# Optimization experiments

Measured on AMD Instinct MI355X. Metric: run time of the kernel, lower is better.

Reference implementation:

```python
import jax, jax.numpy as jnp
import numpy as np

N_HIDDEN = 100  # module-level global n_hidden in source
LN_EPS = 1e-5


def _layernorm(x, g, b):
    mu = jnp.mean(x, axis=-1, keepdims=True)
    var = jnp.mean(jnp.square(x - mu), axis=-1, keepdims=True)
    return (x - mu) * jax.lax.rsqrt(var + LN_EPS) * g + b


def setup_inputs() -> dict:
    key = jax.random.key(0)
    B, T, C, H = 8, 1024, 768, 12
    D = C // H  # head_size = 64
    ks = jax.random.split(key, 12)
    s_qkv = 1.0 / np.sqrt(C)
    s_ff1 = 1.0 / np.sqrt(C)
    s_ff2 = 1.0 / np.sqrt(N_HIDDEN)
    return {
        "x": jax.random.normal(ks[0], (B, T, C), dtype=jnp.float32),
        # per-head K/Q/V projections stacked: [H, C, D]
        "Wq": jax.random.uniform(ks[1], (H, C, D), jnp.float32, -s_qkv, s_qkv),
        "Wk": jax.random.uniform(ks[2], (H, C, D), jnp.float32, -s_qkv, s_qkv),
        "Wv": jax.random.uniform(ks[3], (H, C, D), jnp.float32, -s_qkv, s_qkv),
        "Wproj": jax.random.uniform(ks[4], (C, C), jnp.float32, -s_qkv, s_qkv),
        "bproj": jnp.zeros((C,), jnp.float32),
        "ln1_g": jnp.ones((C,), jnp.float32),
        "ln1_b": jnp.zeros((C,), jnp.float32),
        "W1": jax.random.uniform(ks[5], (C, N_HIDDEN), jnp.float32, -s_ff1, s_ff1),
        "b1": jnp.zeros((N_HIDDEN,), jnp.float32),
        "W2": jax.random.uniform(ks[6], (N_HIDDEN, C), jnp.float32, -s_ff2, s_ff2),
        "b2": jnp.zeros((C,), jnp.float32),
        "ln2_g": jnp.ones((C,), jnp.float32),
        "ln2_b": jnp.zeros((C,), jnp.float32),
    }


def reference(x, Wq, Wk, Wv, Wproj, bproj, ln1_g, ln1_b, W1, b1, W2, b2, ln2_g, ln2_b):
    B, T, C = x.shape
    # batched-over-heads QKV (source does a Python loop per head; same math)
    q = jnp.einsum('btc,hcd->bhtd', x, Wq)
    k = jnp.einsum('btc,hcd->bhtd', x, Wk)
    v = jnp.einsum('btc,hcd->bhtd', x, Wv)
    # NOTE: source scales by C**-0.5 where C = n_embd (not head_size)
    wei = jnp.einsum('bhtd,bhsd->bhts', q, k) * (C ** -0.5)
    wei = jax.nn.softmax(wei, axis=-1)  # attn_maps, returned
    out = jnp.einsum('bhts,bhsd->bhtd', wei, v)
    out = out.transpose(0, 2, 1, 3).reshape(B, T, C)  # concat heads
    attn_out = out @ Wproj + bproj
    h = _layernorm(x + attn_out, ln1_g, ln1_b)
    ff = jax.nn.relu(h @ W1 + b1) @ W2 + b2
    y = _layernorm(h + ff, ln2_g, ln2_b)
    return (wei, y)
```

## Files before the change

### kernel.cpp

```cpp
#include <hip/hip_runtime.h>
#include <hip/hip_bf16.h>
#include <cstdint>

typedef __bf16 bf16_t;
typedef __bf16 bf16x8 __attribute__((ext_vector_type(8)));
typedef __bf16 bf16x4 __attribute__((ext_vector_type(4)));
typedef float f32x4 __attribute__((ext_vector_type(4)));

#define B_ 8
#define T_ 1024
#define C_ 768
#define H_ 12
#define D_ 64
#define NTOK 8192
#define NHID_PAD 128
#define SCALE 0.03608439182435161f
#define WEI_ELEMS 100663296ull

__device__ __forceinline__ f32x4 mfma16(bf16x8 a, bf16x8 b, f32x4 c) {
    return __builtin_amdgcn_mfma_f32_16x16x32_bf16(a, b, c, 0, 0, 0);
}

typedef const unsigned int __attribute__((address_space(1)))* gaddr_t;
typedef unsigned int __attribute__((address_space(3)))* laddr_t;
__device__ __forceinline__ void gload16(const bf16_t* g, bf16_t* l) {
    __builtin_amdgcn_global_load_lds((gaddr_t)g, (laddr_t)l, 16, 0, 0);
}

__global__ __launch_bounds__(256) void k_cast_x(const float* __restrict__ x,
                                                bf16_t* __restrict__ xb) {
    int i = blockIdx.x * 256 + threadIdx.x;
    const float4 v = reinterpret_cast<const float4*>(x)[i];
    bf16x4 o;
    o.x = (bf16_t)v.x; o.y = (bf16_t)v.y; o.z = (bf16_t)v.z; o.w = (bf16_t)v.w;
    *reinterpret_cast<bf16x4*>(xb + 4 * i) = o;
}

__global__ __launch_bounds__(256) void k_pack_qkv(const float* __restrict__ Wq,
                                                  const float* __restrict__ Wk,
                                                  const float* __restrict__ Wv,
                                                  bf16_t* __restrict__ out) {
    int idx = blockIdx.x * 256 + threadIdx.x;
    int row = idx / C_, c = idx - row * C_;
    int p = row / C_;
    int hd = row - p * C_;
    int h = hd >> 6, d = hd & 63;
    const float* W = (p == 0) ? Wq : (p == 1 ? Wk : Wv);
    out[idx] = (bf16_t)W[((size_t)h * C_ + c) * D_ + d];
}

__global__ __launch_bounds__(256) void k_pack_proj(const float* __restrict__ W,
                                                   bf16_t* __restrict__ out) {
    int idx = blockIdx.x * 256 + threadIdx.x;
    int n = idx / C_, k = idx - n * C_;
    out[idx] = (bf16_t)W[(size_t)k * C_ + n];
}

__global__ __launch_bounds__(256) void k_pack_w1(const float* __restrict__ W,
                                                 bf16_t* __restrict__ out) {
    int idx = blockIdx.x * 256 + threadIdx.x;
    int n = idx / C_, k = idx - n * C_;
    out[idx] = (bf16_t)((n < 100) ? W[(size_t)k * 100 + n] : 0.0f);
}

__global__ __launch_bounds__(256) void k_pack_w2(const float* __restrict__ W,
                                                 bf16_t* __restrict__ out) {
    int idx = blockIdx.x * 256 + threadIdx.x;
    int n = idx / NHID_PAD, k = idx & (NHID_PAD - 1);
    out[idx] = (bf16_t)((k < 100) ? W[(size_t)k * C_ + n] : 0.0f);
}

__device__ __forceinline__ void gemm_core(const bf16_t* __restrict__ A, int lda,
                                          const bf16_t* __restrict__ B, int ldb,
                                          int K, f32x4 acc[4][4]) {
    __shared__ __align__(16) bf16_t As[128 * 32];
    __shared__ __align__(16) bf16_t Bs[128 * 32];
    const int tid = threadIdx.x;
    const int wave = tid >> 6, lane = tid & 63;
    const int q = lane >> 4, ln = lane & 15;
    const int wm = (wave >> 1) * 64, wn = (wave & 1) * 64;
    const size_t bm = (size_t)blockIdx.y * 128, bn = (size_t)blockIdx.x * 128;

    const int c0 = wave * 2;
    const int srow = c0 * 16 + (lane >> 2);
    const int kg = (lane & 3) * 8;
    const bf16_t* Ap0 = A + (bm + srow) * lda + kg;
    const bf16_t* Ap1 = A + (bm + srow + 16) * lda + kg;
    const bf16_t* Bp0 = B + (bn + srow) * ldb + kg;
    const bf16_t* Bp1 = B + (bn + srow + 16) * ldb + kg;
    bf16_t* AsD0 = As + c0 * 512;
    bf16_t* AsD1 = As + (c0 + 1) * 512;
    bf16_t* BsD0 = Bs + c0 * 512;
    bf16_t* BsD1 = Bs + (c0 + 1) * 512;

    for (int k0 = 0; k0 < K; k0 += 32) {
        __syncthreads();
        gload16(Ap0 + k0, AsD0);
        gload16(Ap1 + k0, AsD1);
        gload16(Bp0 + k0, BsD0);
        gload16(Bp1 + k0, BsD1);
        __syncthreads();
        bf16x8 af[4], bfr[4];
#pragma unroll
        for (int i = 0; i < 4; ++i)
            af[i] = *reinterpret_cast<const bf16x8*>(&As[(wm + i * 16 + ln) * 32 + q * 8]);
#pragma unroll
        for (int j = 0; j < 4; ++j)
            bfr[j] = *reinterpret_cast<const bf16x8*>(&Bs[(wn + j * 16 + ln) * 32 + q * 8]);
#pragma unroll
        for (int i = 0; i < 4; ++i)
#pragma unroll
            for (int j = 0; j < 4; ++j)
                acc[i][j] = mfma16(af[i], bfr[j], acc[i][j]);
    }
}

#define EPI_PROLOG                                              \
    const int lane = threadIdx.x & 63;                          \
    const int wave = threadIdx.x >> 6;                          \
    const int q = lane >> 4, ln = lane & 15;                    \
    const int row0 = blockIdx.y * 128 + (wave >> 1) * 64;       \
    const int col0 = blockIdx.x * 128 + (wave & 1) * 64;

__global__ __launch_bounds__(256) void k_gemm_qk(const bf16_t* __restrict__ A,
                                                 const bf16_t* __restrict__ Bm,
                                                 bf16_t* __restrict__ qb,
                                                 bf16_t* __restrict__ kb) {
    f32x4 acc[4][4] = {};
    gemm_core(A, C_, Bm, C_, C_, acc);
    EPI_PROLOG
#pragma unroll
    for (int i = 0; i < 4; ++i)
#pragma unroll
        for (int j = 0; j < 4; ++j)
#pragma unroll
            for (int r = 0; r < 4; ++r) {
                int grow = row0 + i * 16 + q * 4 + r;
                int gcol = col0 + j * 16 + ln;
                int p = (gcol >= C_) ? 1 : 0;
                int c = gcol - p * C_;
                int h = c >> 6, d = c & 63;
                int b = grow >> 10, t = grow & 1023;
                bf16_t* dst = p ? kb : qb;
                dst[(((size_t)b * H_ + h) * T_ + t) * D_ + d] = (bf16_t)acc[i][j][r];
            }
}

__global__ __launch_bounds__(256) void k_gemm_vt(const bf16_t* __restrict__ A,
                                                 const bf16_t* __restrict__ Bm,
                                                 bf16_t* __restrict__ vt) {
    f32x4 acc[4][4] = {};
    gemm_core(A, C_, Bm, C_, C_, acc);
    EPI_PROLOG
#pragma unroll
    for (int i = 0; i < 4; ++i)
#pragma unroll
        for (int j = 0; j < 4; ++j)
#pragma unroll
            for (int r = 0; r < 4; ++r) {
                int grow = row0 + i * 16 + q * 4 + r;
                int gcol = col0 + j * 16 + ln;
                int h = grow >> 6, d = grow & 63;
                int b = gcol >> 10, t = gcol & 1023;
                vt[(((size_t)b * H_ + h) * D_ + d) * T_ + t] = (bf16_t)acc[i][j][r];
            }
}

__global__ __launch_bounds__(256) void k_gemm_proj(const bf16_t* __restrict__ A,
                                                   const bf16_t* __restrict__ Bm,
                                                   const float* __restrict__ bias,
                                                   float* __restrict__ out) {
    f32x4 acc[4][4] = {};
    gemm_core(A, C_, Bm, C_, C_, acc);
    EPI_PROLOG
#pragma unroll
    for (int i = 0; i < 4; ++i)
#pragma unroll
        for (int j = 0; j < 4; ++j)
#pragma unroll
            for (int r = 0; r < 4; ++r) {
                int grow = row0 + i * 16 + q * 4 + r;
                int gcol = col0 + j * 16 + ln;
                out[(size_t)grow * C_ + gcol] = acc[i][j][r] + bias[gcol];
            }
}

__global__ __launch_bounds__(256) void k_gemm_ff1(const bf16_t* __restrict__ A,
                                                  const bf16_t* __restrict__ Bm,
                                                  const float* __restrict__ bias,
                                                  bf16_t* __restrict__ out) {
    f32x4 acc[4][4] = {};
    gemm_core(A, C_, Bm, C_, C_, acc);
    EPI_PROLOG
#pragma unroll
    for (int i = 0; i < 4; ++i)
#pragma unroll
        for (int j = 0; j < 4; ++j)
#pragma unroll
            for (int r = 0; r < 4; ++r) {
                int grow = row0 + i * 16 + q * 4 + r;
                int gcol = col0 + j * 16 + ln;
                float v = acc[i][j][r] + ((gcol < 100) ? bias[gcol] : 0.0f);
                v = fmaxf(v, 0.0f);
                out[(size_t)grow * NHID_PAD + gcol] = (bf16_t)v;
            }
}

__global__ __launch_bounds__(256) void k_gemm_ff2(const bf16_t* __restrict__ A,
                                                  const bf16_t* __restrict__ Bm,
                                                  const float* __restrict__ bias,
                                                  float* __restrict__ out) {
    f32x4 acc[4][4] = {};
    gemm_core(A, NHID_PAD, Bm, NHID_PAD, NHID_PAD, acc);
    EPI_PROLOG
#pragma unroll
    for (int i = 0; i < 4; ++i)
#pragma unroll
        for (int j = 0; j < 4; ++j)
#pragma unroll
            for (int r = 0; r < 4; ++r) {
                int grow = row0 + i * 16 + q * 4 + r;
                int gcol = col0 + j * 16 + ln;
                out[(size_t)grow * C_ + gcol] = acc[i][j][r] + bias[gcol];
            }
}

__global__ __launch_bounds__(256, 3) void k_attn(const bf16_t* __restrict__ qb,
                                                 const bf16_t* __restrict__ kb,
                                                 const bf16_t* __restrict__ vt,
                                                 float* __restrict__ wei,
                                                 bf16_t* __restrict__ attn) {
    __shared__ __align__(16) bf16_t Ps[16 * 1032];
    __shared__ float redm[4][16];
    __shared__ float reds[4][16];

    const int tid = threadIdx.x;
    const int w = tid >> 6, lane = tid & 63;
    const int qq = lane >> 4, ln = lane & 15;
    const int bh = blockIdx.y;
    const int b = bh / H_, h = bh - b * H_;
    const int t0 = blockIdx.x * 16;
    const size_t bhbase = (size_t)bh * (T_ * D_);

    const bf16_t* qp = qb + bhbase + (size_t)(t0 + ln) * D_ + qq * 8;
    const bf16x8 aq0 = *reinterpret_cast<const bf16x8*>(qp);
    const bf16x8 aq1 = *reinterpret_cast<const bf16x8*>(qp + 32);

    f32x4 sacc[16] = {};
    const bf16_t* kp = kb + bhbase + (size_t)(w * 256 + ln) * D_ + qq * 8;
#pragma unroll
    for (int j = 0; j < 16; ++j) {
        bf16x8 b0 = *reinterpret_cast<const bf16x8*>(kp + j * 16 * D_);
        bf16x8 b1 = *reinterpret_cast<const bf16x8*>(kp + j * 16 * D_ + 32);
        sacc[j] = mfma16(aq0, b0, sacc[j]);
        sacc[j] = mfma16(aq1, b1, sacc[j]);
    }

    float mx[4];
#pragma unroll
    for (int r = 0; r < 4; ++r) {
        float m = sacc[0][r];
#pragma unroll
        for (int j = 1; j < 16; ++j) m = fmaxf(m, sacc[j][r]);
#pragma unroll
        for (int off = 1; off < 16; off <<= 1) m = fmaxf(m, __shfl_xor(m, off));
        mx[r] = m;
    }
    if (ln == 0) {
#pragma unroll
        for (int r = 0; r < 4; ++r) redm[w][qq * 4 + r] = mx[r];
    }
    __syncthreads();
#pragma unroll
    for (int r = 0; r < 4; ++r) {
        int row = qq * 4 + r;
        mx[r] = fmaxf(fmaxf(redm[0][row], redm[1][row]),
                      fmaxf(redm[2][row], redm[3][row]));
    }

    float rs[4] = {0.0f, 0.0f, 0.0f, 0.0f};
#pragma unroll
    for (int j = 0; j < 16; ++j)
#pragma unroll
        for (int r = 0; r < 4; ++r) {
            float p = __expf((sacc[j][r] - mx[r]) * SCALE);
            sacc[j][r] = p;
            rs[r] += p;
        }
#pragma unroll
    for (int r = 0; r < 4; ++r)
#pragma unroll
        for (int off = 1; off < 16; off <<= 1) rs[r] += __shfl_xor(rs[r], off);
    if (ln == 0) {
#pragma unroll
        for (int r = 0; r < 4; ++r) reds[w][qq * 4 + r] = rs[r];
    }
    __syncthreads();
    float inv[4];
#pragma unroll
    for (int r = 0; r < 4; ++r) {
        int row = qq * 4 + r;
        inv[r] = 1.0f / (reds[0][row] + reds[1][row] + reds[2][row] + reds[3][row]);
    }

    float* wbase = wei + ((size_t)bh << 20) + (size_t)t0 * T_ + w * 256 + ln;
#pragma unroll
    for (int r = 0; r < 4; ++r) {
        int row = qq * 4 + r;
        float* wr = wbase + (size_t)row * T_;
        bf16_t* pr = &Ps[row * 1032 + w * 256 + ln];
#pragma unroll
        for (int j = 0; j < 16; ++j) {
            float p = sacc[j][r] * inv[r];
            wr[j * 16] = p;
            pr[j * 16] = (bf16_t)p;
        }
    }
    __syncthreads();

    f32x4 oacc = {};
    const bf16_t* vp = vt + (size_t)bh * (D_ * T_) + (size_t)(w * 16 + ln) * T_ + qq * 8;
#pragma unroll
    for (int ks = 0; ks < 32; ++ks) {
        bf16x8 a = *reinterpret_cast<const bf16x8*>(&Ps[ln * 1032 + ks * 32 + qq * 8]);
        bf16x8 bv = *reinterpret_cast<const bf16x8*>(vp + ks * 32);
        oacc = mfma16(a, bv, oacc);
    }
#pragma unroll
    for (int r = 0; r < 4; ++r) {
        int trow = t0 + qq * 4 + r;
        attn[((size_t)b * T_ + trow) * C_ + h * D_ + w * 16 + ln] = (bf16_t)oacc[r];
    }
}

__global__ __launch_bounds__(256) void k_ln(const float* __restrict__ a,
                                            const float* __restrict__ bsrc,
                                            const float* __restrict__ g,
                                            const float* __restrict__ beta,
                                            float* __restrict__ of,
                                            bf16_t* __restrict__ ob) {
    int row = blockIdx.x;
    int tid = threadIdx.x;
    const float* pa = a + (size_t)row * C_;
    const float* pb = bsrc + (size_t)row * C_;
    float v[3];
    float s = 0.0f, s2 = 0.0f;
#pragma unroll
    for (int u = 0; u < 3; ++u) {
        int c = tid + u * 256;
        v[u] = pa[c] + pb[c];
        s += v[u];
        s2 += v[u] * v[u];
    }
#pragma unroll
    for (int off = 32; off; off >>= 1) {
        s += __shfl_down(s, off);
        s2 += __shfl_down(s2, off);
    }
    __shared__ float ws[4], ws2[4];
    if ((tid & 63) == 0) { ws[tid >> 6] = s; ws2[tid >> 6] = s2; }
    __syncthreads();
    s = ws[0] + ws[1] + ws[2] + ws[3];
    s2 = ws2[0] + ws2[1] + ws2[2] + ws2[3];
    float mu = s * (1.0f / C_);
    float var = s2 * (1.0f / C_) - mu * mu;
    float ri = rsqrtf(var + 1e-5f);
#pragma unroll
    for (int u = 0; u < 3; ++u) {
        int c = tid + u * 256;
        float y = (v[u] - mu) * ri * g[c] + beta[c];
        of[(size_t)row * C_ + c] = y;
        if (ob) ob[(size_t)row * C_ + c] = (bf16_t)y;
    }
}

extern "C" void kernel_launch(void* const* d_in, const int* in_sizes, int n_in,
                              void* d_out, int out_size, void* d_ws, size_t ws_size,
                              hipStream_t stream) {
    const float* x     = (const float*)d_in[0];
    const float* Wq    = (const float*)d_in[1];
    const float* Wk    = (const float*)d_in[2];
    const float* Wv    = (const float*)d_in[3];
    const float* Wproj = (const float*)d_in[4];
    const float* bproj = (const float*)d_in[5];
    const float* ln1g  = (const float*)d_in[6];
    const float* ln1b  = (const float*)d_in[7];
    const float* W1    = (const float*)d_in[8];
    const float* b1    = (const float*)d_in[9];
    const float* W2    = (const float*)d_in[10];
    const float* b2    = (const float*)d_in[11];
    const float* ln2g  = (const float*)d_in[12];
    const float* ln2b  = (const float*)d_in[13];

    char* ws = (char*)d_ws;
    bf16_t* xb     = (bf16_t*)(ws + 0);
    bf16_t* wqkvt  = (bf16_t*)(ws + 12582912);
    bf16_t* qbuf   = (bf16_t*)(ws + 16121856);
    bf16_t* kbuf   = (bf16_t*)(ws + 28704768);
    bf16_t* vtb    = (bf16_t*)(ws + 41287680);
    bf16_t* attnb  = (bf16_t*)(ws + 53870592);
    bf16_t* wprojt = (bf16_t*)(ws + 66453504);
    float*  projb  = (float*)(ws + 67633152);
    float*  hbuf   = (float*)(ws + 92798976);
    bf16_t* hidb   = (bf16_t*)(ws + 117964800);
    bf16_t* w1t    = (bf16_t*)(ws + 120061952);
    bf16_t* w2t    = (bf16_t*)(ws + 120258560);
    bf16_t* hbb    = xb;
    float*  ffb    = projb;

    float* wei = (float*)d_out;
    float* y   = (float*)d_out + WEI_ELEMS;

    k_cast_x<<<6144, 256, 0, stream>>>(x, xb);
    k_pack_qkv<<<6912, 256, 0, stream>>>(Wq, Wk, Wv, wqkvt);
    k_pack_proj<<<2304, 256, 0, stream>>>(Wproj, wprojt);
    k_pack_w1<<<384, 256, 0, stream>>>(W1, w1t);
    k_pack_w2<<<384, 256, 0, stream>>>(W2, w2t);

    k_gemm_qk<<<dim3(12, 64), 256, 0, stream>>>(xb, wqkvt, qbuf, kbuf);
    k_gemm_vt<<<dim3(64, 6), 256, 0, stream>>>(wqkvt + (size_t)1536 * C_, xb, vtb);

    k_attn<<<dim3(64, 96), 256, 0, stream>>>(qbuf, kbuf, vtb, wei, attnb);

    k_gemm_proj<<<dim3(6, 64), 256, 0, stream>>>(attnb, wprojt, bproj, projb);
    k_ln<<<8192, 256, 0, stream>>>(x, projb, ln1g, ln1b, hbuf, hbb);
    k_gemm_ff1<<<dim3(1, 64), 256, 0, stream>>>(hbb, w1t, b1, hidb);
    k_gemm_ff2<<<dim3(6, 64), 256, 0, stream>>>(hidb, w2t, b2, ffb);
    k_ln<<<8192, 256, 0, stream>>>(hbuf, ffb, ln2g, ln2b, y, (bf16_t*)nullptr);

    (void)in_sizes; (void)n_in; (void)out_size; (void)ws_size;
}
```

Before: 765.3 us.

## Merge prep and QKV launches, double-buffer GEMM core, fuse FFN, add nontemporal stores

Merges the five cast/pack kernels into one launch and the QK and V^T GEMMs into a single 1D-grid launch. Gives the shared GEMM core LDS double buffering so the next K-tile load is issued before the current tile's MFMAs. Fuses FF1 and FF2 into one kernel that keeps the ReLU hidden tile in swizzled LDS; each block recomputes FF1 for three column groups. Switches the large attention-weight output and the final LayerNorm output to nontemporal stores to reduce cache pollution.

```diff
diff --git a/kernel.cpp b/kernel.cpp
--- a/kernel.cpp
+++ b/kernel.cpp
@@ -27,152 +27,160 @@
     __builtin_amdgcn_global_load_lds((gaddr_t)g, (laddr_t)l, 16, 0, 0);
 }
 
-__global__ __launch_bounds__(256) void k_cast_x(const float* __restrict__ x,
-                                                bf16_t* __restrict__ xb) {
-    int i = blockIdx.x * 256 + threadIdx.x;
-    const float4 v = reinterpret_cast<const float4*>(x)[i];
-    bf16x4 o;
-    o.x = (bf16_t)v.x; o.y = (bf16_t)v.y; o.z = (bf16_t)v.z; o.w = (bf16_t)v.w;
-    *reinterpret_cast<bf16x4*>(xb + 4 * i) = o;
-}
-
-__global__ __launch_bounds__(256) void k_pack_qkv(const float* __restrict__ Wq,
-                                                  const float* __restrict__ Wk,
-                                                  const float* __restrict__ Wv,
-                                                  bf16_t* __restrict__ out) {
-    int idx = blockIdx.x * 256 + threadIdx.x;
-    int row = idx / C_, c = idx - row * C_;
-    int p = row / C_;
-    int hd = row - p * C_;
-    int h = hd >> 6, d = hd & 63;
-    const float* W = (p == 0) ? Wq : (p == 1 ? Wk : Wv);
-    out[idx] = (bf16_t)W[((size_t)h * C_ + c) * D_ + d];
-}
-
-__global__ __launch_bounds__(256) void k_pack_proj(const float* __restrict__ W,
-                                                   bf16_t* __restrict__ out) {
-    int idx = blockIdx.x * 256 + threadIdx.x;
-    int n = idx / C_, k = idx - n * C_;
-    out[idx] = (bf16_t)W[(size_t)k * C_ + n];
-}
-
-__global__ __launch_bounds__(256) void k_pack_w1(const float* __restrict__ W,
-                                                 bf16_t* __restrict__ out) {
-    int idx = blockIdx.x * 256 + threadIdx.x;
-    int n = idx / C_, k = idx - n * C_;
-    out[idx] = (bf16_t)((n < 100) ? W[(size_t)k * 100 + n] : 0.0f);
-}
-
-__global__ __launch_bounds__(256) void k_pack_w2(const float* __restrict__ W,
-                                                 bf16_t* __restrict__ out) {
-    int idx = blockIdx.x * 256 + threadIdx.x;
-    int n = idx / NHID_PAD, k = idx & (NHID_PAD - 1);
-    out[idx] = (bf16_t)((k < 100) ? W[(size_t)k * C_ + n] : 0.0f);
-}
-
-__device__ __forceinline__ void gemm_core(const bf16_t* __restrict__ A, int lda,
+__global__ __launch_bounds__(256) void k_prep(const float* __restrict__ x, bf16_t* __restrict__ xb,
+                                              const float* __restrict__ Wq, const float* __restrict__ Wk,
+                                              const float* __restrict__ Wv, bf16_t* __restrict__ wqkvt,
+                                              const float* __restrict__ Wproj, bf16_t* __restrict__ wprojt,
+                                              const float* __restrict__ W1, bf16_t* __restrict__ w1t,
+                                              const float* __restrict__ W2, bf16_t* __restrict__ w2t) {
+    int blk = blockIdx.x;
+    int tid = threadIdx.x;
+    if (blk < 6144) {
+        int i = blk * 256 + tid;
+        const float4 v = reinterpret_cast<const float4*>(x)[i];
+        bf16x4 o;
+        o.x = (bf16_t)v.x; o.y = (bf16_t)v.y; o.z = (bf16_t)v.z; o.w = (bf16_t)v.w;
+        *reinterpret_cast<bf16x4*>(xb + 4 * i) = o;
+    } else if (blk < 13056) {
+        int idx = (blk - 6144) * 256 + tid;
+        int row = idx / C_, c = idx - row * C_;
+        int p = row / C_;
+        int hd = row - p * C_;
+        int h = hd >> 6, d = hd & 63;
+        const float* W = (p == 0) ? Wq : (p == 1 ? Wk : Wv);
+        wqkvt[idx] = (bf16_t)W[((size_t)h * C_ + c) * D_ + d];
+    } else if (blk < 15360) {
+        int idx = (blk - 13056) * 256 + tid;
+        int n = idx / C_, k = idx - n * C_;
+        wprojt[idx] = (bf16_t)Wproj[(size_t)k * C_ + n];
+    } else if (blk < 15744) {
+        int idx = (blk - 15360) * 256 + tid;
+        int n = idx / C_, k = idx - n * C_;
+        w1t[idx] = (bf16_t)((n < 100) ? W1[(size_t)k * 100 + n] : 0.0f);
+    } else {
+        int idx = (blk - 15744) * 256 + tid;
+        int n = idx / NHID_PAD, k = idx & (NHID_PAD - 1);
+        w2t[idx] = (bf16_t)((k < 100) ? W2[(size_t)k * C_ + n] : 0.0f);
+    }
+}
+
+__device__ __forceinline__ void gemm_core(bf16_t* As, bf16_t* Bs,
+                                          const bf16_t* __restrict__ A, int lda,
                                           const bf16_t* __restrict__ B, int ldb,
-                                          int K, f32x4 acc[4][4]) {
-    __shared__ __align__(16) bf16_t As[128 * 32];
-    __shared__ __align__(16) bf16_t Bs[128 * 32];
+                                          int K, int bm, int bn, f32x4 acc[4][4]) {
     const int tid = threadIdx.x;
     const int wave = tid >> 6, lane = tid & 63;
     const int q = lane >> 4, ln = lane & 15;
     const int wm = (wave >> 1) * 64, wn = (wave & 1) * 64;
-    const size_t bm = (size_t)blockIdx.y * 128, bn = (size_t)blockIdx.x * 128;
 
     const int c0 = wave * 2;
     const int srow = c0 * 16 + (lane >> 2);
     const int kg = (lane & 3) * 8;
-    const bf16_t* Ap0 = A + (bm + srow) * lda + kg;
-    const bf16_t* Ap1 = A + (bm + srow + 16) * lda + kg;
-    const bf16_t* Bp0 = B + (bn + srow) * ldb + kg;
-    const bf16_t* Bp1 = B + (bn + srow + 16) * ldb + kg;
-    bf16_t* AsD0 = As + c0 * 512;
-    bf16_t* AsD1 = As + (c0 + 1) * 512;
-    bf16_t* BsD0 = Bs + c0 * 512;
-    bf16_t* BsD1 = Bs + (c0 + 1) * 512;
-
-    for (int k0 = 0; k0 < K; k0 += 32) {
+    const bf16_t* Ap0 = A + (size_t)(bm + srow) * lda + kg;
+    const bf16_t* Ap1 = A + (size_t)(bm + srow + 16) * lda + kg;
+    const bf16_t* Bp0 = B + (size_t)(bn + srow) * ldb + kg;
+    const bf16_t* Bp1 = B + (size_t)(bn + srow + 16) * ldb + kg;
+
+    const int nt = K >> 5;
+    gload16(Ap0, As + c0 * 512);
+    gload16(Ap1, As + (c0 + 1) * 512);
+    gload16(Bp0, Bs + c0 * 512);
+    gload16(Bp1, Bs + (c0 + 1) * 512);
+    int cur = 0;
+    for (int t = 0; t < nt; ++t) {
         __syncthreads();
-        gload16(Ap0 + k0, AsD0);
-        gload16(Ap1 + k0, AsD1);
-        gload16(Bp0 + k0, BsD0);
-        gload16(Bp1 + k0, BsD1);
-        __syncthreads();
+        if (t + 1 < nt) {
+            int k0 = (t + 1) << 5;
+            bf16_t* Ad = As + (cur ^ 1) * 4096;
+            bf16_t* Bd = Bs + (cur ^ 1) * 4096;
+            gload16(Ap0 + k0, Ad + c0 * 512);
+            gload16(Ap1 + k0, Ad + (c0 + 1) * 512);
+            gload16(Bp0 + k0, Bd + c0 * 512);
+            gload16(Bp1 + k0, Bd + (c0 + 1) * 512);
+        }
+        const bf16_t* Ab = As + cur * 4096;
+        const bf16_t* Bb = Bs + cur * 4096;
         bf16x8 af[4], bfr[4];
 #pragma unroll
         for (int i = 0; i < 4; ++i)
-            af[i] = *reinterpret_cast<const bf16x8*>(&As[(wm + i * 16 + ln) * 32 + q * 8]);
+            af[i] = *reinterpret_cast<const bf16x8*>(&Ab[(wm + i * 16 + ln) * 32 + q * 8]);
 #pragma unroll
         for (int j = 0; j < 4; ++j)
-            bfr[j] = *reinterpret_cast<const bf16x8*>(&Bs[(wn + j * 16 + ln) * 32 + q * 8]);
+            bfr[j] = *reinterpret_cast<const bf16x8*>(&Bb[(wn + j * 16 + ln) * 32 + q * 8]);
 #pragma unroll
         for (int i = 0; i < 4; ++i)
 #pragma unroll
             for (int j = 0; j < 4; ++j)
                 acc[i][j] = mfma16(af[i], bfr[j], acc[i][j]);
-    }
-}
-
-#define EPI_PROLOG                                              \
+        cur ^= 1;
+    }
+}
+
+#define EPI_PROLOG(bm, bn)                                      \
     const int lane = threadIdx.x & 63;                          \
     const int wave = threadIdx.x >> 6;                          \
     const int q = lane >> 4, ln = lane & 15;                    \
-    const int row0 = blockIdx.y * 128 + (wave >> 1) * 64;       \
-    const int col0 = blockIdx.x * 128 + (wave & 1) * 64;
-
-__global__ __launch_bounds__(256) void k_gemm_qk(const bf16_t* __restrict__ A,
-                                                 const bf16_t* __restrict__ Bm,
-                                                 bf16_t* __restrict__ qb,
-                                                 bf16_t* __restrict__ kb) {
-    f32x4 acc[4][4] = {};
-    gemm_core(A, C_, Bm, C_, C_, acc);
-    EPI_PROLOG
-#pragma unroll
-    for (int i = 0; i < 4; ++i)
-#pragma unroll
-        for (int j = 0; j < 4; ++j)
-#pragma unroll
-            for (int r = 0; r < 4; ++r) {
-                int grow = row0 + i * 16 + q * 4 + r;
-                int gcol = col0 + j * 16 + ln;
-                int p = (gcol >= C_) ? 1 : 0;
-                int c = gcol - p * C_;
-                int h = c >> 6, d = c & 63;
-                int b = grow >> 10, t = grow & 1023;
-                bf16_t* dst = p ? kb : qb;
-                dst[(((size_t)b * H_ + h) * T_ + t) * D_ + d] = (bf16_t)acc[i][j][r];
-            }
-}
-
-__global__ __launch_bounds__(256) void k_gemm_vt(const bf16_t* __restrict__ A,
-                                                 const bf16_t* __restrict__ Bm,
-                                                 bf16_t* __restrict__ vt) {
-    f32x4 acc[4][4] = {};
-    gemm_core(A, C_, Bm, C_, C_, acc);
-    EPI_PROLOG
-#pragma unroll
-    for (int i = 0; i < 4; ++i)
-#pragma unroll
-        for (int j = 0; j < 4; ++j)
-#pragma unroll
-            for (int r = 0; r < 4; ++r) {
-                int grow = row0 + i * 16 + q * 4 + r;
-                int gcol = col0 + j * 16 + ln;
-                int h = grow >> 6, d = grow & 63;
-                int b = gcol >> 10, t = gcol & 1023;
-                vt[(((size_t)b * H_ + h) * D_ + d) * T_ + t] = (bf16_t)acc[i][j][r];
-            }
+    const int row0 = (bm) + (wave >> 1) * 64;                   \
+    const int col0 = (bn) + (wave & 1) * 64;
+
+__global__ __launch_bounds__(256) void k_gemm_qkv(const bf16_t* __restrict__ xb,
+                                                  const bf16_t* __restrict__ wqkvt,
+                                                  bf16_t* __restrict__ qb,
+                                                  bf16_t* __restrict__ kb,
+                                                  bf16_t* __restrict__ vt) {
+    __shared__ __align__(16) bf16_t As[2 * 4096];
+    __shared__ __align__(16) bf16_t Bs[2 * 4096];
+    const int bid = blockIdx.x;
+    if (bid < 768) {
+        const int bx = bid % 12, by = bid / 12;
+        f32x4 acc[4][4] = {};
+        gemm_core(As, Bs, xb, C_, wqkvt, C_, C_, by * 128, bx * 128, acc);
+        EPI_PROLOG(by * 128, bx * 128)
+#pragma unroll
+        for (int i = 0; i < 4; ++i)
+#pragma unroll
+            for (int j = 0; j < 4; ++j)
+#pragma unroll
+                for (int r = 0; r < 4; ++r) {
+                    int grow = row0 + i * 16 + q * 4 + r;
+                    int gcol = col0 + j * 16 + ln;
+                    int p = (gcol >= C_) ? 1 : 0;
+                    int c = gcol - p * C_;
+                    int h = c >> 6, d = c & 63;
+                    int b = grow >> 10, t = grow & 1023;
+                    bf16_t* dst = p ? kb : qb;
+                    dst[(((size_t)b * H_ + h) * T_ + t) * D_ + d] = (bf16_t)acc[i][j][r];
+                }
+    } else {
+        const int b2 = bid - 768;
+        const int bx = b2 & 63, by = b2 >> 6;
+        f32x4 acc[4][4] = {};
+        gemm_core(As, Bs, wqkvt + (size_t)1536 * C_, C_, xb, C_, C_, by * 128, bx * 128, acc);
+        EPI_PROLOG(by * 128, bx * 128)
+#pragma unroll
+        for (int i = 0; i < 4; ++i)
+#pragma unroll
+            for (int j = 0; j < 4; ++j)
+#pragma unroll
+                for (int r = 0; r < 4; ++r) {
+                    int grow = row0 + i * 16 + q * 4 + r;
+                    int gcol = col0 + j * 16 + ln;
+                    int h = grow >> 6, d = grow & 63;
+                    int b = gcol >> 10, t = gcol & 1023;
+                    vt[(((size_t)b * H_ + h) * D_ + d) * T_ + t] = (bf16_t)acc[i][j][r];
+                }
+    }
 }
 
 __global__ __launch_bounds__(256) void k_gemm_proj(const bf16_t* __restrict__ A,
                                                    const bf16_t* __restrict__ Bm,
                                                    const float* __restrict__ bias,
                                                    float* __restrict__ out) {
+    __shared__ __align__(16) bf16_t As[2 * 4096];
+    __shared__ __align__(16) bf16_t Bs[2 * 4096];
     f32x4 acc[4][4] = {};
-    gemm_core(A, C_, Bm, C_, C_, acc);
-    EPI_PROLOG
+    gemm_core(As, Bs, A, C_, Bm, C_, C_, blockIdx.y * 128, blockIdx.x * 128, acc);
+    EPI_PROLOG(blockIdx.y * 128, blockIdx.x * 128)
 #pragma unroll
     for (int i = 0; i < 4; ++i)
 #pragma unroll
@@ -185,44 +193,71 @@
             }
 }
 
-__global__ __launch_bounds__(256) void k_gemm_ff1(const bf16_t* __restrict__ A,
-                                                  const bf16_t* __restrict__ Bm,
-                                                  const float* __restrict__ bias,
-                                                  bf16_t* __restrict__ out) {
+__global__ __launch_bounds__(256) void k_ff(const bf16_t* __restrict__ hbb,
+                                            const bf16_t* __restrict__ w1t,
+                                            const float* __restrict__ b1,
+                                            const bf16_t* __restrict__ w2t,
+                                            const float* __restrict__ b2,
+                                            float* __restrict__ out) {
+    __shared__ __align__(16) bf16_t As[2 * 4096];
+    __shared__ __align__(16) bf16_t Bs[2 * 4096];
+    __shared__ __align__(16) bf16_t Hs[128 * 128];
+    const int bm = blockIdx.y * 128;
     f32x4 acc[4][4] = {};
-    gemm_core(A, C_, Bm, C_, C_, acc);
-    EPI_PROLOG
+    gemm_core(As, Bs, hbb, C_, w1t, C_, C_, bm, 0, acc);
+
+    const int tid = threadIdx.x;
+    const int wave = tid >> 6, lane = tid & 63;
+    const int q = lane >> 4, ln = lane & 15;
+    const int wm = (wave >> 1) * 64, wn = (wave & 1) * 64;
 #pragma unroll
     for (int i = 0; i < 4; ++i)
 #pragma unroll
         for (int j = 0; j < 4; ++j)
 #pragma unroll
             for (int r = 0; r < 4; ++r) {
-                int grow = row0 + i * 16 + q * 4 + r;
-                int gcol = col0 + j * 16 + ln;
-                float v = acc[i][j][r] + ((gcol < 100) ? bias[gcol] : 0.0f);
+                int row = wm + i * 16 + q * 4 + r;
+                int col = wn + j * 16 + ln;
+                float v = acc[i][j][r] + ((col < 100) ? b1[col] : 0.0f);
                 v = fmaxf(v, 0.0f);
-                out[(size_t)grow * NHID_PAD + gcol] = (bf16_t)v;
+                Hs[(row * 128 + col) ^ ((row & 7) << 3)] = (bf16_t)v;
             }
-}
-
-__global__ __launch_bounds__(256) void k_gemm_ff2(const bf16_t* __restrict__ A,
-                                                  const bf16_t* __restrict__ Bm,
-                                                  const float* __restrict__ bias,
-                                                  float* __restrict__ out) {
-    f32x4 acc[4][4] = {};
-    gemm_core(A, NHID_PAD, Bm, NHID_PAD, NHID_PAD, acc);
-    EPI_PROLOG
-#pragma unroll
-    for (int i = 0; i < 4; ++i)
-#pragma unroll
-        for (int j = 0; j < 4; ++j)
-#pragma unroll
-            for (int r = 0; r < 4; ++r) {
-                int grow = row0 + i * 16 + q * 4 + r;
-                int gcol = col0 + j * 16 + ln;
-                out[(size_t)grow * C_ + gcol] = acc[i][j][r] + bias[gcol];
+    __syncthreads();
+
+#pragma unroll
+    for (int nt2 = 0; nt2 < 2; ++nt2) {
+        const int cb = blockIdx.x * 256 + nt2 * 128;
+        f32x4 a2[4][4] = {};
+#pragma unroll
+        for (int k0 = 0; k0 < 128; k0 += 32) {
+            bf16x8 af[4], bfr[4];
+#pragma unroll
+            for (int i = 0; i < 4; ++i) {
+                int row = wm + i * 16 + ln;
+                af[i] = *reinterpret_cast<const bf16x8*>(
+                    &Hs[(row * 128 + k0 + q * 8) ^ ((row & 7) << 3)]);
             }
+#pragma unroll
+            for (int j = 0; j < 4; ++j)
+                bfr[j] = *reinterpret_cast<const bf16x8*>(
+                    &w2t[(size_t)(cb + wn + j * 16 + ln) * NHID_PAD + k0 + q * 8]);
+#pragma unroll
+            for (int i = 0; i < 4; ++i)
+#pragma unroll
+                for (int j = 0; j < 4; ++j)
+                    a2[i][j] = mfma16(af[i], bfr[j], a2[i][j]);
+        }
+#pragma unroll
+        for (int i = 0; i < 4; ++i)
+#pragma unroll
+            for (int j = 0; j < 4; ++j)
+#pragma unroll
+                for (int r = 0; r < 4; ++r) {
+                    int grow = bm + wm + i * 16 + q * 4 + r;
+                    int gcol = cb + wn + j * 16 + ln;
+                    out[(size_t)grow * C_ + gcol] = a2[i][j][r] + b2[gcol];
+                }
+    }
 }
 
 __global__ __launch_bounds__(256, 3) void k_attn(const bf16_t* __restrict__ qb,
@@ -312,7 +347,7 @@
 #pragma unroll
         for (int j = 0; j < 16; ++j) {
             float p = sacc[j][r] * inv[r];
-            wr[j * 16] = p;
+            __builtin_nontemporal_store(p, wr + j * 16);
             pr[j * 16] = (bf16_t)p;
         }
     }
@@ -338,7 +373,8 @@
                                             const float* __restrict__ g,
                                             const float* __restrict__ beta,
                                             float* __restrict__ of,
-                                            bf16_t* __restrict__ ob) {
+                                            bf16_t* __restrict__ ob,
+                                            int streaming) {
     int row = blockIdx.x;
     int tid = threadIdx.x;
     const float* pa = a + (size_t)row * C_;
@@ -369,7 +405,8 @@
     for (int u = 0; u < 3; ++u) {
         int c = tid + u * 256;
         float y = (v[u] - mu) * ri * g[c] + beta[c];
-        of[(size_t)row * C_ + c] = y;
+        if (streaming) __builtin_nontemporal_store(y, &of[(size_t)row * C_ + c]);
+        else of[(size_t)row * C_ + c] = y;
         if (ob) ob[(size_t)row * C_ + c] = (bf16_t)y;
     }
 }
@@ -402,7 +439,6 @@
     bf16_t* wprojt = (bf16_t*)(ws + 66453504);
     float*  projb  = (float*)(ws + 67633152);
     float*  hbuf   = (float*)(ws + 92798976);
-    bf16_t* hidb   = (bf16_t*)(ws + 117964800);
     bf16_t* w1t    = (bf16_t*)(ws + 120061952);
     bf16_t* w2t    = (bf16_t*)(ws + 120258560);
     bf16_t* hbb    = xb;
@@ -411,22 +447,14 @@
     float* wei = (float*)d_out;
     float* y   = (float*)d_out + WEI_ELEMS;
 
-    k_cast_x<<<6144, 256, 0, stream>>>(x, xb);
-    k_pack_qkv<<<6912, 256, 0, stream>>>(Wq, Wk, Wv, wqkvt);
-    k_pack_proj<<<2304, 256, 0, stream>>>(Wproj, wprojt);
-    k_pack_w1<<<384, 256, 0, stream>>>(W1, w1t);
-    k_pack_w2<<<384, 256, 0, stream>>>(W2, w2t);
-
-    k_gemm_qk<<<dim3(12, 64), 256, 0, stream>>>(xb, wqkvt, qbuf, kbuf);
-    k_gemm_vt<<<dim3(64, 6), 256, 0, stream>>>(wqkvt + (size_t)1536 * C_, xb, vtb);
-
+    k_prep<<<16128, 256, 0, stream>>>(x, xb, Wq, Wk, Wv, wqkvt, Wproj, wprojt,
+                                      W1, w1t, W2, w2t);
+    k_gemm_qkv<<<1152, 256, 0, stream>>>(xb, wqkvt, qbuf, kbuf, vtb);
     k_attn<<<dim3(64, 96), 256, 0, stream>>>(qbuf, kbuf, vtb, wei, attnb);
-
     k_gemm_proj<<<dim3(6, 64), 256, 0, stream>>>(attnb, wprojt, bproj, projb);
-    k_ln<<<8192, 256, 0, stream>>>(x, projb, ln1g, ln1b, hbuf, hbb);
-    k_gemm_ff1<<<dim3(1, 64), 256, 0, stream>>>(hbb, w1t, b1, hidb);
-    k_gemm_ff2<<<dim3(6, 64), 256, 0, stream>>>(hidb, w2t, b2, ffb);
-    k_ln<<<8192, 256, 0, stream>>>(hbuf, ffb, ln2g, ln2b, y, (bf16_t*)nullptr);
+    k_ln<<<8192, 256, 0, stream>>>(x, projb, ln1g, ln1b, hbuf, hbb, 0);
+    k_ff<<<dim3(3, 64), 256, 0, stream>>>(hbb, w1t, b1, w2t, b2, ffb);
+    k_ln<<<8192, 256, 0, stream>>>(hbuf, ffb, ln2g, ln2b, y, (bf16_t*)nullptr, 1);
 
     (void)in_sizes; (void)n_in; (void)out_size; (void)ws_size;
 }
```

Result: faster. 726.5 us (-5.1%).
